# Kernel optimization log

Measured on AMD Instinct MI355X. Metric: run time of the kernel, lower is better.

Reference implementation:

```python
import math
import jax, jax.numpy as jnp
import numpy as np

B, S, D, H = 2, 2048, 1024, 16
Dh = D // H
EPS = 1e-5


def layernorm(x, g, b):
    mu = jnp.mean(x, axis=-1, keepdims=True)
    var = jnp.mean(jnp.square(x - mu), axis=-1, keepdims=True)
    return (x - mu) * jax.lax.rsqrt(var + EPS) * g + b


def setup_inputs() -> dict:
    key = jax.random.key(0)
    ks = jax.random.split(key, 8)
    sc = 0.02
    return {
        "x": jax.random.normal(ks[0], (B, S, D), jnp.float32),
        # per-head wq weights stacked: [H, D, Dh] (wk/wv are unused in the original)
        "wq_w": jax.random.normal(ks[1], (H, D, Dh), jnp.float32) * sc,
        "wq_b": jnp.zeros((H, Dh), jnp.float32),
        "fc_w": jax.random.normal(ks[2], (D, D), jnp.float32) * sc,
        "fc_b": jnp.zeros((D,), jnp.float32),
        "ln1_g": jnp.ones((D,), jnp.float32),
        "ln1_b": jnp.zeros((D,), jnp.float32),
        "w1": jax.random.normal(ks[3], (D, 4 * D), jnp.float32) * sc,
        "b1": jnp.zeros((4 * D,), jnp.float32),
        "w2": jax.random.normal(ks[4], (4 * D, D), jnp.float32) * sc,
        "b2": jnp.zeros((D,), jnp.float32),
        "ln2_g": jnp.ones((D,), jnp.float32),
        "ln2_b": jnp.zeros((D,), jnp.float32),
    }


def reference(x, wq_w, wq_b, fc_w, fc_b, ln1_g, ln1_b, w1, b1, w2, b2, ln2_g, ln2_b):
    # NOTE: original bug — wq is applied to q, k and v; since q=k=v=x, Q=K=V.
    qh = jnp.einsum("bsd,hde->bhse", x, wq_w) + wq_b[None, :, None, :]  # [B,H,S,Dh]
    scores = jnp.einsum("bhse,bhte->bhst", qh, qh) / math.sqrt(Dh)      # [B,H,S,S]
    attn = jax.nn.softmax(scores, axis=-1)
    ctx = jnp.einsum("bhst,bhte->bhse", attn, qh)                        # [B,H,S,Dh]
    # concat heads along last dim (head h -> columns h*Dh:(h+1)*Dh)
    y = jnp.transpose(ctx, (0, 2, 1, 3)).reshape(B, S, D)
    y = y @ fc_w + fc_b
    y = layernorm(y + x, ln1_g, ln1_b)
    y1 = jax.nn.relu(y @ w1 + b1) @ w2 + b2
    return layernorm(y + y1, ln2_g, ln2_b)
```

## Files before the change

kernel.cpp:

```cpp
#include <hip/hip_runtime.h>
#include <hip/hip_bf16.h>

typedef unsigned short u16;
typedef __bf16 bf16x8 __attribute__((ext_vector_type(8)));
typedef float floatx4 __attribute__((ext_vector_type(4)));

__device__ __forceinline__ float bf2f_u(u16 u) {
    union { unsigned int i; float f; } x; x.i = ((unsigned int)u) << 16; return x.f;
}
__device__ __forceinline__ u16 f2bf_u(float f) {
    union { float f; unsigned int i; } x; x.f = f;
    unsigned int r = x.i + 0x7fffu + ((x.i >> 16) & 1u);
    return (u16)(r >> 16);
}

__device__ __forceinline__ void gl_lds16(const void* g, void* l) {
    __builtin_amdgcn_global_load_lds(
        (const __attribute__((address_space(1))) void*)g,
        (__attribute__((address_space(3))) void*)l, 16, 0, 0);
}

__device__ __forceinline__ void transpose_body(
    const float* __restrict__ ip, u16* __restrict__ op,
    int R, int C, int r0, int c0, int t, u16 (*T)[80])
{
#pragma unroll
    for (int i = 0; i < 4; i++) {
        int c = t + i * 256;
        int rr = c >> 4, cc = (c & 15) * 4;
        float4 v = *(const float4*)&ip[(size_t)(r0 + rr) * C + c0 + cc];
        T[cc + 0][rr] = f2bf_u(v.x); T[cc + 1][rr] = f2bf_u(v.y);
        T[cc + 2][rr] = f2bf_u(v.z); T[cc + 3][rr] = f2bf_u(v.w);
    }
    __syncthreads();
#pragma unroll
    for (int i = 0; i < 2; i++) {
        int c = t + i * 256;
        int oc = c >> 3, k8 = (c & 7) * 8;
        uint4 v = *(const uint4*)&T[oc][k8];
        *(uint4*)&op[(size_t)(c0 + oc) * R + r0 + k8] = v;
    }
}

__global__ __launch_bounds__(256) void prep_k(
    const float* __restrict__ x,    u16* __restrict__ x_bf,
    const float* __restrict__ w1,   u16* __restrict__ w1_bt,
    const float* __restrict__ w2,   u16* __restrict__ w2_bt,
    const float* __restrict__ wq_w, u16* __restrict__ wqm_bt,
    const float* __restrict__ fc_w, u16* __restrict__ fcw_bt)
{
    __shared__ u16 T[64][80];
    const int id = blockIdx.x, t = threadIdx.x;
    if (id < 2048) {
        int i = (id * 256 + t) * 8;
        float4 v0 = *(const float4*)&x[i];
        float4 v1 = *(const float4*)&x[i + 4];
        u16 tmp[8] = {f2bf_u(v0.x), f2bf_u(v0.y), f2bf_u(v0.z), f2bf_u(v0.w),
                      f2bf_u(v1.x), f2bf_u(v1.y), f2bf_u(v1.z), f2bf_u(v1.w)};
        *(uint4*)&x_bf[i] = *(const uint4*)tmp;
    } else if (id < 3072) {
        int j = id - 2048;
        transpose_body(w1, w1_bt, 1024, 4096, (j >> 6) * 64, (j & 63) * 64, t, T);
    } else if (id < 4096) {
        int j = id - 3072;
        transpose_body(w2, w2_bt, 4096, 1024, (j >> 4) * 64, (j & 15) * 64, t, T);
    } else if (id < 4352) {
        int j = id - 4096;
        int z = j >> 4;
        transpose_body(wq_w + (size_t)z * (1024 * 64),
                       wqm_bt + (size_t)z * (64 * 1024),
                       1024, 64, (j & 15) * 64, 0, t, T);
    } else {
        int j = id - 4352;
        transpose_body(fc_w, fcw_bt, 1024, 1024, (j >> 4) * 64, (j & 15) * 64, t, T);
    }
}

__global__ __launch_bounds__(256) void transpose_qh_k(const u16* __restrict__ in,
                                                      u16* __restrict__ out)
{
    __shared__ u16 T[64][72];
    const int bh = blockIdx.y;
    const int s0 = blockIdx.x * 64;
    const u16* ip = in + (size_t)bh * (2048 * 64);
    u16* op = out + (size_t)bh * (64 * 2048);
    const int t = threadIdx.x;
#pragma unroll
    for (int i = 0; i < 2; i++) {
        int c = t + i * 256;
        int r = c >> 3, cc = (c & 7) * 8;
        uint4 v = *(const uint4*)&ip[(size_t)(s0 + r) * 64 + cc];
        const u16* pv = (const u16*)&v;
#pragma unroll
        for (int k = 0; k < 8; k++) T[cc + k][r] = pv[k];
    }
    __syncthreads();
#pragma unroll
    for (int i = 0; i < 2; i++) {
        int c = t + i * 256;
        int d = c >> 3, cs = (c & 7) * 8;
        uint4 v = *(const uint4*)&T[d][cs];
        *(uint4*)&op[(size_t)d * 2048 + s0 + cs] = v;
    }
}

__device__ __forceinline__ void gemm_epilogue(
    floatx4 (&acc)[4][2], int m0, int n0, int wm, int wn, int lr, int quad,
    int N, const float* __restrict__ bias, const u16* __restrict__ resid,
    float* __restrict__ out, u16* __restrict__ out_bf, int mode)
{
#pragma unroll
    for (int i = 0; i < 4; i++) {
#pragma unroll
        for (int j = 0; j < 2; j++) {
#pragma unroll
            for (int r = 0; r < 4; r++) {
                int grow = m0 + wm + i * 16 + quad * 4 + r;
                int gcol = n0 + wn + j * 16 + lr;
                float val = acc[i][j][r];
                if (bias) val += bias[gcol];
                if (mode == 0) {
                    int bb = grow >> 11, ss = grow & 2047;
                    int h = gcol >> 6, e = gcol & 63;
                    out_bf[(((size_t)bb * 16 + h) * 2048 + ss) * 64 + e] = f2bf_u(val);
                } else if (mode == 1) {
                    size_t idx = (size_t)grow * N + gcol;
                    out[idx] = val + bf2f_u(resid[idx]);
                } else if (mode == 2) {
                    out_bf[(size_t)grow * N + gcol] = f2bf_u(fmaxf(val, 0.f));
                } else if (mode == 3) {
                    size_t idx = (size_t)grow * N + gcol;
                    out[idx] = out[idx] + val;
                } else {
                    size_t idx = (size_t)grow * N + gcol;
                    out_bf[idx] = f2bf_u(val + bf2f_u(resid[idx]));
                }
            }
        }
    }
}

__global__ __launch_bounds__(256) void gemm_bt64p3_k(
    const u16* __restrict__ A, const u16* __restrict__ Bt,
    int gm, int gn, int N, int K, int ldb,
    const float* __restrict__ bias, const u16* __restrict__ resid,
    float* __restrict__ out, u16* __restrict__ out_bf, int mode)
{
    __shared__ __align__(16) u16 As[3][128 * 64];
    __shared__ __align__(16) u16 Bs[3][64 * 64];

    const int id = blockIdx.x;
    const int xcd = id & 7, s = id >> 3;
    const int bandM = gm >> 2, bandN = gn >> 1;
    const int m0 = ((xcd >> 1) * bandM + (s % bandM)) * 128;
    const int n0 = ((xcd & 1) * bandN + (s / bandM)) * 64;

    const int t = threadIdx.x;
    const int wid = t >> 6, lane = t & 63;
    const int wm = (wid >> 1) * 64, wn = (wid & 1) * 32;
    const int lr = lane & 15, quad = lane >> 4;
    const int srow = lane >> 3;
    const int scol = ((lane & 7) ^ (lane >> 3)) * 8;

    floatx4 acc[4][2];
#pragma unroll
    for (int i = 0; i < 4; i++)
#pragma unroll
        for (int j = 0; j < 2; j++)
            acc[i][j] = (floatx4){0.f, 0.f, 0.f, 0.f};

    auto stage = [&](int b, int k0) {
#pragma unroll
        for (int i = 0; i < 4; i++) {
            int rb = wid * 32 + i * 8;
            gl_lds16(&A[(size_t)(m0 + rb + srow) * K + k0 + scol], &As[b][rb * 64]);
        }
#pragma unroll
        for (int i = 0; i < 2; i++) {
            int rb = wid * 16 + i * 8;
            gl_lds16(&Bt[(size_t)(n0 + rb + srow) * ldb + k0 + scol], &Bs[b][rb * 64]);
        }
    };

    const int nt = K >> 6;
    stage(0, 0);
    stage(1, 64);

    int cur = 0, nxt = 2;
    for (int tt = 0; tt < nt; tt++) {
        if (tt + 1 < nt) asm volatile("s_waitcnt vmcnt(6)" ::: "memory");
        else             asm volatile("s_waitcnt vmcnt(0)" ::: "memory");
        __builtin_amdgcn_s_barrier();
        __builtin_amdgcn_sched_barrier(0);
        if (tt + 2 < nt) stage(nxt, (tt + 2) * 64);

#pragma unroll
        for (int kk = 0; kk < 2; kk++) {
            bf16x8 af[4], bfr[2];
#pragma unroll
            for (int i = 0; i < 4; i++) {
                int R = wm + i * 16 + lr;
                int c = ((kk * 4 + quad) ^ (lr & 7)) * 8;
                af[i] = *(const bf16x8*)&As[cur][R * 64 + c];
            }
#pragma unroll
            for (int j = 0; j < 2; j++) {
                int R = wn + j * 16 + lr;
                int c = ((kk * 4 + quad) ^ (lr & 7)) * 8;
                bfr[j] = *(const bf16x8*)&Bs[cur][R * 64 + c];
            }
#pragma unroll
            for (int i = 0; i < 4; i++)
#pragma unroll
                for (int j = 0; j < 2; j++)
                    acc[i][j] = __builtin_amdgcn_mfma_f32_16x16x32_bf16(af[i], bfr[j], acc[i][j], 0, 0, 0);
        }
        cur = (cur == 2) ? 0 : cur + 1;
        nxt = (nxt == 2) ? 0 : nxt + 1;
    }

    gemm_epilogue(acc, m0, n0, wm, wn, lr, quad, N, bias, resid, out, out_bf, mode);
}

__global__ __launch_bounds__(256) void gemm_bt64m_k(
    const u16* __restrict__ A, const u16* __restrict__ Bt,
    int gm, int gn, int N, int K, int ldb,
    const float* __restrict__ bias, const u16* __restrict__ resid,
    float* __restrict__ out, u16* __restrict__ out_bf, int mode)
{
    __shared__ __align__(16) u16 As[2][64 * 64];
    __shared__ __align__(16) u16 Bs[2][64 * 64];

    const int id = blockIdx.x;
    const int xcd = id & 7, s = id >> 3;
    const int bandM = gm >> 2, bandN = gn >> 1;
    const int m0 = ((xcd >> 1) * bandM + (s % bandM)) * 64;
    const int n0 = ((xcd & 1) * bandN + (s / bandM)) * 64;

    const int t = threadIdx.x;
    const int wid = t >> 6, lane = t & 63;
    const int wm = (wid >> 1) * 32, wn = (wid & 1) * 32;
    const int lr = lane & 15, quad = lane >> 4;
    const int srow = lane >> 3;
    const int scol = ((lane & 7) ^ (lane >> 3)) * 8;

    floatx4 acc[2][2];
#pragma unroll
    for (int i = 0; i < 2; i++)
#pragma unroll
        for (int j = 0; j < 2; j++)
            acc[i][j] = (floatx4){0.f, 0.f, 0.f, 0.f};

    auto stage = [&](int b, int k0) {
#pragma unroll
        for (int i = 0; i < 2; i++) {
            int rb = wid * 16 + i * 8;
            gl_lds16(&A[(size_t)(m0 + rb + srow) * K + k0 + scol], &As[b][rb * 64]);
        }
#pragma unroll
        for (int i = 0; i < 2; i++) {
            int rb = wid * 16 + i * 8;
            gl_lds16(&Bt[(size_t)(n0 + rb + srow) * ldb + k0 + scol], &Bs[b][rb * 64]);
        }
    };

    const int nt = K >> 6;
    stage(0, 0);

    int cur = 0;
    for (int tt = 0; tt < nt; tt++) {
        asm volatile("s_waitcnt vmcnt(0)" ::: "memory");
        __builtin_amdgcn_s_barrier();
        __builtin_amdgcn_sched_barrier(0);
        if (tt + 1 < nt) stage(cur ^ 1, (tt + 1) * 64);

#pragma unroll
        for (int kk = 0; kk < 2; kk++) {
            bf16x8 af[2], bfr[2];
#pragma unroll
            for (int i = 0; i < 2; i++) {
                int R = wm + i * 16 + lr;
                int c = ((kk * 4 + quad) ^ (lr & 7)) * 8;
                af[i] = *(const bf16x8*)&As[cur][R * 64 + c];
            }
#pragma unroll
            for (int j = 0; j < 2; j++) {
                int R = wn + j * 16 + lr;
                int c = ((kk * 4 + quad) ^ (lr & 7)) * 8;
                bfr[j] = *(const bf16x8*)&Bs[cur][R * 64 + c];
            }
#pragma unroll
            for (int i = 0; i < 2; i++)
#pragma unroll
                for (int j = 0; j < 2; j++)
                    acc[i][j] = __builtin_amdgcn_mfma_f32_16x16x32_bf16(af[i], bfr[j], acc[i][j], 0, 0, 0);
        }
        cur ^= 1;
    }

#pragma unroll
    for (int i = 0; i < 2; i++) {
#pragma unroll
        for (int j = 0; j < 2; j++) {
#pragma unroll
            for (int r = 0; r < 4; r++) {
                int grow = m0 + wm + i * 16 + quad * 4 + r;
                int gcol = n0 + wn + j * 16 + lr;
                float val = acc[i][j][r];
                if (bias) val += bias[gcol];
                if (mode == 1) {
                    size_t idx = (size_t)grow * N + gcol;
                    out[idx] = val + bf2f_u(resid[idx]);
                } else if (mode == 3) {
                    size_t idx = (size_t)grow * N + gcol;
                    out[idx] = out[idx] + val;
                } else {
                    out_bf[(size_t)grow * N + gcol] = f2bf_u(fmaxf(val, 0.f));
                }
            }
        }
    }
}

#define PST 68
__global__ __launch_bounds__(256) void attn_mfma_k(const u16* __restrict__ qh,
                                                   const u16* __restrict__ qhT,
                                                   u16* __restrict__ ctx)
{
    __shared__ __align__(16) u16 Ks[2][64 * 64];
    __shared__ __align__(16) u16 Vt[2][64 * 64];
    __shared__ __align__(16) u16 Ps[4][2][16][PST];

    const int bh = blockIdx.x >> 4;
    const int qb = blockIdx.x & 15;
    const u16* __restrict__ base  = qh  + (size_t)bh * (2048 * 64);
    const u16* __restrict__ baseT = qhT + (size_t)bh * (64 * 2048);
    const int t = threadIdx.x, wid = t >> 6, lane = t & 63;
    const int lr = lane & 15, quad = lane >> 4;
    const int q0 = qb * 128 + wid * 16;

    bf16x8 af[2][2];
#pragma unroll
    for (int f = 0; f < 2; f++) {
        af[f][0] = *(const bf16x8*)&base[(size_t)(q0 + f * 64 + lr) * 64 + quad * 8];
        af[f][1] = *(const bf16x8*)&base[(size_t)(q0 + f * 64 + lr) * 64 + quad * 8 + 32];
    }

    floatx4 Of[2][4];
#pragma unroll
    for (int f = 0; f < 2; f++)
#pragma unroll
        for (int dt = 0; dt < 4; dt++) Of[f][dt] = (floatx4){0.f, 0.f, 0.f, 0.f};
    float lsum[2] = {0.f, 0.f};

    const int srow = lane >> 3;
    const int schk = (lane & 7) ^ srow;

    auto stage = [&](int b, int kt) {
#pragma unroll
        for (int i = 0; i < 2; i++) {
            int rb = (wid * 2 + i) * 8;
            gl_lds16(&base[(size_t)(kt + rb + srow) * 64 + schk * 8],
                     &Ks[b][rb * 64]);
            gl_lds16(&baseT[(size_t)(rb + srow) * 2048 + kt + schk * 8],
                     &Vt[b][rb * 64]);
        }
    };

    stage(0, 0);
    __syncthreads();

    int buf = 0;
    for (int kt = 0; kt < 2048; kt += 64) {
        if (kt + 64 < 2048) stage(buf ^ 1, kt + 64);

#pragma unroll
        for (int nt = 0; nt < 4; nt++) {
            int row = nt * 16 + lr, rsw = row & 7;
            bf16x8 b0 = *(const bf16x8*)&Ks[buf][row * 64 + ((quad ^ rsw) * 8)];
            bf16x8 b1 = *(const bf16x8*)&Ks[buf][row * 64 + (((quad + 4) ^ rsw) * 8)];
#pragma unroll
            for (int f = 0; f < 2; f++) {
                floatx4 z = (floatx4){0.f, 0.f, 0.f, 0.f};
                z = __builtin_amdgcn_mfma_f32_16x16x32_bf16(b0, af[f][0], z, 0, 0, 0);
                z = __builtin_amdgcn_mfma_f32_16x16x32_bf16(b1, af[f][1], z, 0, 0, 0);
                float p0 = __expf(fminf(z[0] * 0.125f, 60.f));
                float p1 = __expf(fminf(z[1] * 0.125f, 60.f));
                float p2 = __expf(fminf(z[2] * 0.125f, 60.f));
                float p3 = __expf(fminf(z[3] * 0.125f, 60.f));
                lsum[f] += (p0 + p1) + (p2 + p3);
                unsigned int lo, hi;
                asm("v_cvt_pk_bf16_f32 %0, %1, %2" : "=v"(lo) : "v"(p0), "v"(p1));
                asm("v_cvt_pk_bf16_f32 %0, %1, %2" : "=v"(hi) : "v"(p2), "v"(p3));
                uint2 pk; pk.x = lo; pk.y = hi;
                *(uint2*)&Ps[wid][f][lr][nt * 16 + quad * 4] = pk;
            }
        }

        bf16x8 aP[2][2];
#pragma unroll
        for (int f = 0; f < 2; f++) {
            aP[f][0] = *(const bf16x8*)&Ps[wid][f][lr][quad * 8];
            aP[f][1] = *(const bf16x8*)&Ps[wid][f][lr][quad * 8 + 32];
        }
        __builtin_amdgcn_s_setprio(1);
#pragma unroll
        for (int dt = 0; dt < 4; dt++) {
            int d = dt * 16 + lr, dsw = d & 7;
            bf16x8 b0 = *(const bf16x8*)&Vt[buf][d * 64 + ((quad ^ dsw) * 8)];
            bf16x8 b1 = *(const bf16x8*)&Vt[buf][d * 64 + (((quad + 4) ^ dsw) * 8)];
#pragma unroll
            for (int f = 0; f < 2; f++) {
                Of[f][dt] = __builtin_amdgcn_mfma_f32_16x16x32_bf16(aP[f][0], b0, Of[f][dt], 0, 0, 0);
                Of[f][dt] = __builtin_amdgcn_mfma_f32_16x16x32_bf16(aP[f][1], b1, Of[f][dt], 0, 0, 0);
            }
        }
        __builtin_amdgcn_s_setprio(0);

        __syncthreads();
        buf ^= 1;
    }

    const int b = bh >> 4, h = bh & 15;
#pragma unroll
    for (int f = 0; f < 2; f++) {
        float l = lsum[f];
        l += __shfl_xor(l, 16);
        l += __shfl_xor(l, 32);
#pragma unroll
        for (int r = 0; r < 4; r++) {
            float lq = __shfl(l, quad * 4 + r);
            float inv = 1.f / lq;
            size_t rowoff = ((size_t)b * 2048 + q0 + f * 64 + quad * 4 + r) * 1024 + h * 64;
#pragma unroll
            for (int dt = 0; dt < 4; dt++)
                ctx[rowoff + dt * 16 + lr] = f2bf_u(Of[f][dt][r] * inv);
        }
    }
}

__global__ __launch_bounds__(256) void ln_k(const void* __restrict__ in,
                                            const float* __restrict__ g,
                                            const float* __restrict__ b,
                                            float* __restrict__ out_f,
                                            u16* __restrict__ out_bf, int icode)
{
    const int row = blockIdx.x;
    const int t = threadIdx.x;
    float4 v;
    if (icode) {
        v = *(const float4*)&((const float*)in)[(size_t)row * 1024 + t * 4];
    } else {
        ushort4 u = *(const ushort4*)&((const u16*)in)[(size_t)row * 1024 + t * 4];
        v.x = bf2f_u(u.x); v.y = bf2f_u(u.y); v.z = bf2f_u(u.z); v.w = bf2f_u(u.w);
    }
    float s  = v.x + v.y + v.z + v.w;
    float ss = v.x * v.x + v.y * v.y + v.z * v.z + v.w * v.w;
#pragma unroll
    for (int off = 32; off >= 1; off >>= 1) {
        s  += __shfl_down(s, off);
        ss += __shfl_down(ss, off);
    }
    __shared__ float sm[10];
    const int wid = t >> 6, lane = t & 63;
    if (lane == 0) { sm[wid] = s; sm[4 + wid] = ss; }
    __syncthreads();
    if (t == 0) {
        float S  = sm[0] + sm[1] + sm[2] + sm[3];
        float SS = sm[4] + sm[5] + sm[6] + sm[7];
        float mu = S * (1.f / 1024.f);
        float var = SS * (1.f / 1024.f) - mu * mu;
        sm[8] = mu; sm[9] = rsqrtf(fmaxf(var, 0.f) + 1e-5f);
    }
    __syncthreads();
    float mu = sm[8], rs = sm[9];
    float4 G  = *(const float4*)&g[t * 4];
    float4 Bv = *(const float4*)&b[t * 4];
    float r0 = (v.x - mu) * rs * G.x + Bv.x;
    float r1 = (v.y - mu) * rs * G.y + Bv.y;
    float r2 = (v.z - mu) * rs * G.z + Bv.z;
    float r3 = (v.w - mu) * rs * G.w + Bv.w;
    if (out_f) {
        float4 ov = {r0, r1, r2, r3};
        *(float4*)&out_f[(size_t)row * 1024 + t * 4] = ov;
    }
    if (out_bf) {
        ushort4 ou = {f2bf_u(r0), f2bf_u(r1), f2bf_u(r2), f2bf_u(r3)};
        *(ushort4*)&out_bf[(size_t)row * 1024 + t * 4] = ou;
    }
}

extern "C" void kernel_launch(void* const* d_in, const int* in_sizes, int n_in,
                              void* d_out, int out_size, void* d_ws, size_t ws_size,
                              hipStream_t stream)
{
    const float* x    = (const float*)d_in[0];
    const float* wq_w = (const float*)d_in[1];
    const float* wq_b = (const float*)d_in[2];
    const float* fc_w = (const float*)d_in[3];
    const float* fc_b = (const float*)d_in[4];
    const float* ln1g = (const float*)d_in[5];
    const float* ln1b = (const float*)d_in[6];
    const float* w1   = (const float*)d_in[7];
    const float* b1   = (const float*)d_in[8];
    const float* w2   = (const float*)d_in[9];
    const float* b2   = (const float*)d_in[10];
    const float* ln2g = (const float*)d_in[11];
    const float* ln2b = (const float*)d_in[12];

    char* ws = (char*)d_ws;
    const size_t MB = 1024 * 1024;
    u16*   w1_bt  = (u16*)(ws);
    u16*   w2_bt  = (u16*)(ws + 8 * MB);
    u16*   wqm_bt = (u16*)(ws + 16 * MB);
    u16*   fcw_bt = (u16*)(ws + 18 * MB);
    u16*   x_bf   = (u16*)(ws + 20 * MB);
    u16*   qh     = (u16*)(ws + 28 * MB);
    u16*   yln1   = (u16*)(ws + 28 * MB);
    u16*   ctx    = (u16*)(ws + 36 * MB);
    u16*   yfc_bf = (u16*)(ws + 44 * MB);
    u16*   qhT    = (u16*)(ws + 44 * MB);
    u16*   h1     = (u16*)(ws + 36 * MB);
    float* z      = (float*)d_out;
    const bool fullN = ws_size >= 69 * MB;

    prep_k<<<4608, 256, 0, stream>>>(x, x_bf, w1, w1_bt, w2, w2_bt,
                                     wq_w, wqm_bt, fc_w, fcw_bt);

    gemm_bt64p3_k<<<512, 256, 0, stream>>>(x_bf, wqm_bt, 32, 16, 1024, 1024, 1024,
                                           wq_b, nullptr, nullptr, qh, 0);
    transpose_qh_k<<<dim3(32, 32), 256, 0, stream>>>(qh, qhT);
    attn_mfma_k<<<512, 256, 0, stream>>>(qh, qhT, ctx);
    gemm_bt64p3_k<<<512, 256, 0, stream>>>(ctx, fcw_bt, 32, 16, 1024, 1024, 1024,
                                           fc_b, x_bf, nullptr, yfc_bf, 4);
    ln_k<<<4096, 256, 0, stream>>>(yfc_bf, ln1g, ln1b, nullptr, yln1, 0);

    if (fullN) {
        gemm_bt64m_k<<<4096, 256, 0, stream>>>(yln1, w1_bt, 64, 64, 4096, 1024, 1024,
                                               b1, nullptr, nullptr, h1, 2);
        gemm_bt64m_k<<<1024, 256, 0, stream>>>(h1, w2_bt, 64, 16, 1024, 4096, 4096,
                                               b2, yln1, z, nullptr, 1);
    } else {
        gemm_bt64m_k<<<2048, 256, 0, stream>>>(yln1, w1_bt, 64, 32, 2048, 1024, 1024,
                                               b1, nullptr, nullptr, h1, 2);
        gemm_bt64m_k<<<1024, 256, 0, stream>>>(h1, w2_bt, 64, 16, 1024, 2048, 4096,
                                               b2, yln1, z, nullptr, 1);
        gemm_bt64m_k<<<2048, 256, 0, stream>>>(yln1, w1_bt + (size_t)2048 * 1024, 64, 32,
                                               2048, 1024, 1024,
                                               b1 + 2048, nullptr, nullptr, h1, 2);
        gemm_bt64m_k<<<1024, 256, 0, stream>>>(h1, w2_bt + 2048, 64, 16, 1024, 2048, 4096,
                                               nullptr, nullptr, z, nullptr, 3);
    }
    ln_k<<<4096, 256, 0, stream>>>(z, ln2g, ln2b, (float*)d_out, nullptr, 1);
}
```

Baseline: 360.9 us.

## Halve query tile per attention block and double grid, use exp2 softmax

Each attention block now handles 64 query rows (one 16-row fragment per wave) instead of 128, and the grid doubles to 1024 blocks. This raises parallelism and cuts per-thread registers and LDS, which can improve occupancy. The cost is that every K/V tile is staged from global memory twice as often. The exponential is also rewritten as exp2f with a prescaled log2e constant.

```diff
diff --git a/kernel.cpp b/kernel.cpp
--- a/kernel.cpp
+++ b/kernel.cpp
@@ -329,29 +329,23 @@
 {
     __shared__ __align__(16) u16 Ks[2][64 * 64];
     __shared__ __align__(16) u16 Vt[2][64 * 64];
-    __shared__ __align__(16) u16 Ps[4][2][16][PST];
-
-    const int bh = blockIdx.x >> 4;
-    const int qb = blockIdx.x & 15;
+    __shared__ __align__(16) u16 Ps[4][16][PST];
+
+    const int bh = blockIdx.x >> 5;
+    const int qb = blockIdx.x & 31;
     const u16* __restrict__ base  = qh  + (size_t)bh * (2048 * 64);
     const u16* __restrict__ baseT = qhT + (size_t)bh * (64 * 2048);
     const int t = threadIdx.x, wid = t >> 6, lane = t & 63;
     const int lr = lane & 15, quad = lane >> 4;
-    const int q0 = qb * 128 + wid * 16;
-
-    bf16x8 af[2][2];
-#pragma unroll
-    for (int f = 0; f < 2; f++) {
-        af[f][0] = *(const bf16x8*)&base[(size_t)(q0 + f * 64 + lr) * 64 + quad * 8];
-        af[f][1] = *(const bf16x8*)&base[(size_t)(q0 + f * 64 + lr) * 64 + quad * 8 + 32];
-    }
-
-    floatx4 Of[2][4];
-#pragma unroll
-    for (int f = 0; f < 2; f++)
-#pragma unroll
-        for (int dt = 0; dt < 4; dt++) Of[f][dt] = (floatx4){0.f, 0.f, 0.f, 0.f};
-    float lsum[2] = {0.f, 0.f};
+    const int q0 = qb * 64 + wid * 16;
+
+    bf16x8 af0 = *(const bf16x8*)&base[(size_t)(q0 + lr) * 64 + quad * 8];
+    bf16x8 af1 = *(const bf16x8*)&base[(size_t)(q0 + lr) * 64 + quad * 8 + 32];
+
+    floatx4 Of[4];
+#pragma unroll
+    for (int dt = 0; dt < 4; dt++) Of[dt] = (floatx4){0.f, 0.f, 0.f, 0.f};
+    float lsum = 0.f;
 
     const int srow = lane >> 3;
     const int schk = (lane & 7) ^ srow;
@@ -370,6 +364,8 @@
     stage(0, 0);
     __syncthreads();
 
+    const float C = 0.18033688011112042f;
+
     int buf = 0;
     for (int kt = 0; kt < 2048; kt += 64) {
         if (kt + 64 < 2048) stage(buf ^ 1, kt + 64);
@@ -379,41 +375,31 @@
             int row = nt * 16 + lr, rsw = row & 7;
             bf16x8 b0 = *(const bf16x8*)&Ks[buf][row * 64 + ((quad ^ rsw) * 8)];
             bf16x8 b1 = *(const bf16x8*)&Ks[buf][row * 64 + (((quad + 4) ^ rsw) * 8)];
-#pragma unroll
-            for (int f = 0; f < 2; f++) {
-                floatx4 z = (floatx4){0.f, 0.f, 0.f, 0.f};
-                z = __builtin_amdgcn_mfma_f32_16x16x32_bf16(b0, af[f][0], z, 0, 0, 0);
-                z = __builtin_amdgcn_mfma_f32_16x16x32_bf16(b1, af[f][1], z, 0, 0, 0);
-                float p0 = __expf(fminf(z[0] * 0.125f, 60.f));
-                float p1 = __expf(fminf(z[1] * 0.125f, 60.f));
-                float p2 = __expf(fminf(z[2] * 0.125f, 60.f));
-                float p3 = __expf(fminf(z[3] * 0.125f, 60.f));
-                lsum[f] += (p0 + p1) + (p2 + p3);
-                unsigned int lo, hi;
-                asm("v_cvt_pk_bf16_f32 %0, %1, %2" : "=v"(lo) : "v"(p0), "v"(p1));
-                asm("v_cvt_pk_bf16_f32 %0, %1, %2" : "=v"(hi) : "v"(p2), "v"(p3));
-                uint2 pk; pk.x = lo; pk.y = hi;
-                *(uint2*)&Ps[wid][f][lr][nt * 16 + quad * 4] = pk;
-            }
-        }
-
-        bf16x8 aP[2][2];
-#pragma unroll
-        for (int f = 0; f < 2; f++) {
-            aP[f][0] = *(const bf16x8*)&Ps[wid][f][lr][quad * 8];
-            aP[f][1] = *(const bf16x8*)&Ps[wid][f][lr][quad * 8 + 32];
-        }
+            floatx4 z = (floatx4){0.f, 0.f, 0.f, 0.f};
+            z = __builtin_amdgcn_mfma_f32_16x16x32_bf16(b0, af0, z, 0, 0, 0);
+            z = __builtin_amdgcn_mfma_f32_16x16x32_bf16(b1, af1, z, 0, 0, 0);
+            float p0 = exp2f(fminf(z[0] * C, 86.56f));
+            float p1 = exp2f(fminf(z[1] * C, 86.56f));
+            float p2 = exp2f(fminf(z[2] * C, 86.56f));
+            float p3 = exp2f(fminf(z[3] * C, 86.56f));
+            lsum += (p0 + p1) + (p2 + p3);
+            unsigned int lo, hi;
+            asm("v_cvt_pk_bf16_f32 %0, %1, %2" : "=v"(lo) : "v"(p0), "v"(p1));
+            asm("v_cvt_pk_bf16_f32 %0, %1, %2" : "=v"(hi) : "v"(p2), "v"(p3));
+            uint2 pk; pk.x = lo; pk.y = hi;
+            *(uint2*)&Ps[wid][lr][nt * 16 + quad * 4] = pk;
+        }
+
+        bf16x8 aP0 = *(const bf16x8*)&Ps[wid][lr][quad * 8];
+        bf16x8 aP1 = *(const bf16x8*)&Ps[wid][lr][quad * 8 + 32];
         __builtin_amdgcn_s_setprio(1);
 #pragma unroll
         for (int dt = 0; dt < 4; dt++) {
             int d = dt * 16 + lr, dsw = d & 7;
             bf16x8 b0 = *(const bf16x8*)&Vt[buf][d * 64 + ((quad ^ dsw) * 8)];
             bf16x8 b1 = *(const bf16x8*)&Vt[buf][d * 64 + (((quad + 4) ^ dsw) * 8)];
-#pragma unroll
-            for (int f = 0; f < 2; f++) {
-                Of[f][dt] = __builtin_amdgcn_mfma_f32_16x16x32_bf16(aP[f][0], b0, Of[f][dt], 0, 0, 0);
-                Of[f][dt] = __builtin_amdgcn_mfma_f32_16x16x32_bf16(aP[f][1], b1, Of[f][dt], 0, 0, 0);
-            }
+            Of[dt] = __builtin_amdgcn_mfma_f32_16x16x32_bf16(aP0, b0, Of[dt], 0, 0, 0);
+            Of[dt] = __builtin_amdgcn_mfma_f32_16x16x32_bf16(aP1, b1, Of[dt], 0, 0, 0);
         }
         __builtin_amdgcn_s_setprio(0);
 
@@ -422,20 +408,17 @@
     }
 
     const int b = bh >> 4, h = bh & 15;
-#pragma unroll
-    for (int f = 0; f < 2; f++) {
-        float l = lsum[f];
-        l += __shfl_xor(l, 16);
-        l += __shfl_xor(l, 32);
-#pragma unroll
-        for (int r = 0; r < 4; r++) {
-            float lq = __shfl(l, quad * 4 + r);
-            float inv = 1.f / lq;
-            size_t rowoff = ((size_t)b * 2048 + q0 + f * 64 + quad * 4 + r) * 1024 + h * 64;
-#pragma unroll
-            for (int dt = 0; dt < 4; dt++)
-                ctx[rowoff + dt * 16 + lr] = f2bf_u(Of[f][dt][r] * inv);
-        }
+    float l = lsum;
+    l += __shfl_xor(l, 16);
+    l += __shfl_xor(l, 32);
+#pragma unroll
+    for (int r = 0; r < 4; r++) {
+        float lq = __shfl(l, quad * 4 + r);
+        float inv = 1.f / lq;
+        size_t rowoff = ((size_t)b * 2048 + q0 + quad * 4 + r) * 1024 + h * 64;
+#pragma unroll
+        for (int dt = 0; dt < 4; dt++)
+            ctx[rowoff + dt * 16 + lr] = f2bf_u(Of[dt][r] * inv);
     }
 }
 
@@ -530,7 +513,7 @@
     gemm_bt64p3_k<<<512, 256, 0, stream>>>(x_bf, wqm_bt, 32, 16, 1024, 1024, 1024,
                                            wq_b, nullptr, nullptr, qh, 0);
     transpose_qh_k<<<dim3(32, 32), 256, 0, stream>>>(qh, qhT);
-    attn_mfma_k<<<512, 256, 0, stream>>>(qh, qhT, ctx);
+    attn_mfma_k<<<1024, 256, 0, stream>>>(qh, qhT, ctx);
     gemm_bt64p3_k<<<512, 256, 0, stream>>>(ctx, fcw_bt, 32, 16, 1024, 1024, 1024,
                                            fc_b, x_bf, nullptr, yfc_bf, 4);
     ln_k<<<4096, 256, 0, stream>>>(yfc_bf, ln1g, ln1b, nullptr, yln1, 0);
```

Measured after the change: 383.9 us. 6.4% more time.
